# Kernel tuning notes

Measured on AMD Instinct MI355X. Metric: run time of the kernel, lower is better.

## Reference

```python
import jax, jax.numpy as jnp
import numpy as np

NUM_CLASSES = 10
EPS = 1e-6


def setup_inputs() -> dict:
    key = jax.random.key(0)
    k1, k2, k3, k4 = jax.random.split(key, 4)
    M, N, D = 4096, 32768, 512
    return {
        "x": jax.random.normal(k1, (M, D), dtype=jnp.float32),
        "x_ref": jax.random.normal(k2, (N, D), dtype=jnp.float32),
        "y": jax.random.randint(k3, (M,), 0, NUM_CLASSES),
        "y_ref": jax.random.randint(k4, (N,), 0, NUM_CLASSES),
    }


def reference(x, x_ref, y, y_ref):
    x2 = jnp.sum(x * x, axis=1)            # [M]
    r2 = jnp.sum(x_ref * x_ref, axis=1)    # [N]
    dist = jnp.sqrt(x2[:, None] - 2.0 * (x @ x_ref.T) + r2[None, :])  # [M,N]
    # scores = -distance, softmax over reference set (temperature = 1)
    score = jax.nn.softmax(-dist, axis=1)  # [M,N]
    # per-class segment sum over reference columns (replaces python loop over 10 classes)
    soft_nns = jax.ops.segment_sum(score.T, y_ref, num_segments=NUM_CLASSES).T + EPS  # [M,10]
    log_soft_nns = jnp.log(soft_nns)
    # nll_loss with reduction='mean'
    loss = -jnp.mean(jnp.take_along_axis(log_soft_nns, y[:, None], axis=1)[:, 0])
    return loss
```

## Files before the change

### kernel.cpp

```cpp
#include <hip/hip_runtime.h>
#include <hip/hip_bf16.h>
#include <stdint.h>

#define M_ROWS 4096
#define N_REFS 32768
#define DIM    512
#define NSPLIT 32
#define BM     128
#define CHUNK  128
#define SLICE  (N_REFS / NSPLIT)
#define NCHUNKS (SLICE / CHUNK)
#define NKT    (DIM / 128)
#define NSTEP  (NCHUNKS * NKT)

typedef __attribute__((ext_vector_type(4))) int   i32x4;
typedef __attribute__((ext_vector_type(8))) int   i32x8;
typedef __attribute__((ext_vector_type(4))) float f32x4;

#define C_L2E2 2.0813689810056077f

__device__ __forceinline__ uint32_t f32_to_e4m3(float f) {
  uint32_t u = __float_as_uint(f);
  uint32_t s = (u >> 24) & 0x80u;
  float a = fabsf(f);
  if (a > 448.f) a = 448.f;
  uint32_t b;
  if (a >= 0.015625f) {
    uint32_t v = __float_as_uint(a);
    v += 0x7FFFFu + ((v >> 20) & 1u);
    int e = (int)(v >> 23) - 127;
    uint32_t m = (v >> 20) & 7u;
    b = (uint32_t)((e + 7) << 3) | m;
    if (b > 0x7Eu) b = 0x7Eu;
  } else {
    b = (uint32_t)(a * 512.f + 0.5f);
  }
  return s | b;
}

__global__ void prep_rows_fp8(const float* __restrict__ src, uint8_t* __restrict__ dst,
                              float* __restrict__ sq) {
  int row = blockIdx.x;
  int t = threadIdx.x;
  const float2* s = (const float2*)(src + (size_t)row * DIM);
  float2 v = s[t];
  uint32_t p = f32_to_e4m3(v.x) | (f32_to_e4m3(v.y) << 8);
  ((uint16_t*)(dst + (size_t)row * DIM))[t] = (uint16_t)p;
  float ss = v.x * v.x + v.y * v.y;
  #pragma unroll
  for (int d = 32; d >= 1; d >>= 1) ss += __shfl_down(ss, d, 64);
  __shared__ float wsum[4];
  int w = t >> 6, lane = t & 63;
  if (lane == 0) wsum[w] = ss;
  __syncthreads();
  if (t == 0) sq[row] = C_L2E2 * (wsum[0] + wsum[1] + wsum[2] + wsum[3]);
}

__global__ __launch_bounds__(256, 2) void ask_main(
    const uint8_t* __restrict__ xf8, const uint8_t* __restrict__ rf8,
    const float* __restrict__ cx2, const float* __restrict__ cr2,
    const int* __restrict__ y, const int* __restrict__ yref,
    float* __restrict__ totG, float* __restrict__ matchG)
{
  __shared__ unsigned char smem[2 * 32768];

  const int tid  = threadIdx.x;
  const int w    = tid >> 6, lane = tid & 63;
  const int wr   = w >> 1,  wc   = w & 1;
  const int l15  = lane & 15, l4 = lane >> 4;

  const int bm       = blockIdx.x * BM;
  const int colstart = blockIdx.y * SLICE;

  const int srow = w * 8 + (lane >> 3);
  const int qsl  = lane & 7;
  const int esl  = qsl ^ (srow & 7);
  const int gsl  = (esl < 4) ? (2 * esl) : (2 * (esl & 3) + 1);
  const int scol = gsl * 16;
  const uint8_t* gA0 = xf8 + (size_t)(bm + srow) * DIM + scol;
  const uint8_t* gBb = rf8 + (size_t)(colstart + srow) * DIM + scol;

#define GLL(srcp, dstoff)                                                        \
  __builtin_amdgcn_global_load_lds(                                              \
      (const __attribute__((address_space(1))) void*)(srcp),                     \
      (__attribute__((address_space(3))) void*)(smem + (dstoff)), 16, 0, 0)

#define STAGE(gidx)                                                              \
  { const int ch_ = (gidx) >> 2, dk_ = ((gidx) & 3) * 128, b_ = ((gidx) & 1) * 32768; \
    const uint8_t* gA_ = gA0 + dk_;                                              \
    const uint8_t* gB_ = gBb + (size_t)ch_ * CHUNK * DIM + dk_;                  \
    _Pragma("unroll")                                                            \
    for (int cc = 0; cc < 4; ++cc) {                                             \
      GLL(gA_ + (size_t)cc * 32 * DIM, b_ + cc * 4096 + w * 1024);               \
      GLL(gB_ + (size_t)cc * 32 * DIM, b_ + 16384 + cc * 4096 + w * 1024);       \
    } }

  const int h   = l15 & 7;
  const int sl0 = (l4 ^ h) * 16;
  const int sl1 = sl0 ^ 64;
  int aoff[4], boff[4];
  #pragma unroll
  for (int i = 0; i < 4; ++i) {
    aoff[i] = (wr * 64 + i * 16 + l15) * 128;
    boff[i] = (wc * 64 + i * 16 + l15) * 128 + 16384;
  }

  float x2v[16]; int yv[16];
  #pragma unroll
  for (int i = 0; i < 16; ++i) {
    int row = bm + wr * 64 + (i >> 2) * 16 + l4 * 4 + (i & 3);
    x2v[i] = cx2[row];
    yv[i]  = y[row];
  }

  float tot[16], mat[16];
  #pragma unroll
  for (int i = 0; i < 16; ++i) { tot[i] = 0.f; mat[i] = 0.f; }

  f32x4 acc[4][4];
  const f32x4 fz = {0.f, 0.f, 0.f, 0.f};

  STAGE(0);
  asm volatile("s_waitcnt vmcnt(0)" ::: "memory");
  __builtin_amdgcn_s_barrier();

  #pragma unroll
  for (int g = 0; g < NSTEP; ++g) {
    const int kt = g & 3, ch = g >> 2;
    const int bofs = (g & 1) * 32768;

    if (g + 1 < NSTEP) { STAGE(g + 1); }

    if (kt == 0) {
      #pragma unroll
      for (int mi = 0; mi < 4; ++mi)
        #pragma unroll
        for (int ni = 0; ni < 4; ++ni) acc[mi][ni] = fz;
    }

    const unsigned char* pS = smem + bofs;
    i32x8 bfr[4];
    #pragma unroll
    for (int ni = 0; ni < 4; ++ni) {
      i32x4 lo = *(const i32x4*)(pS + boff[ni] + sl0);
      i32x4 hi = *(const i32x4*)(pS + boff[ni] + sl1);
      bfr[ni] = __builtin_shufflevector(lo, hi, 0, 1, 2, 3, 4, 5, 6, 7);
    }
    #pragma unroll
    for (int mi = 0; mi < 4; ++mi) {
      i32x4 lo = *(const i32x4*)(pS + aoff[mi] + sl0);
      i32x4 hi = *(const i32x4*)(pS + aoff[mi] + sl1);
      i32x8 afr = __builtin_shufflevector(lo, hi, 0, 1, 2, 3, 4, 5, 6, 7);
      #pragma unroll
      for (int ni = 0; ni < 4; ++ni)
        acc[mi][ni] = __builtin_amdgcn_mfma_scale_f32_16x16x128_f8f6f4(
            afr, bfr[ni], acc[mi][ni],
            0, 0,
            0, 0x7F7F7F7F,
            0, 0x7F7F7F7F);
    }

    if (kt == 3) {
      const int colb = colstart + ch * CHUNK;
      float r2c[4]; int cls[4];
      #pragma unroll
      for (int ni = 0; ni < 4; ++ni) {
        int cg = colb + wc * 64 + ni * 16 + l15;
        r2c[ni] = cr2[cg];
        cls[ni] = yref[cg];
      }
      #pragma unroll
      for (int mi = 0; mi < 4; ++mi) {
        #pragma unroll
        for (int r = 0; r < 4; ++r) {
          const int gi = mi * 4 + r;
          float xr = x2v[gi];
          int   yy = yv[gi];
          float tsum = 0.f, msum = 0.f;
          #pragma unroll
          for (int ni = 0; ni < 4; ++ni) {
            float t = fmaf(-2.0f * C_L2E2, acc[mi][ni][r], xr + r2c[ni]);
            t = fmaxf(t, 0.0f);
            float d = __builtin_amdgcn_sqrtf(t);
            float e = __builtin_amdgcn_exp2f(-d);
            tsum += e;
            msum = fmaf(e, (cls[ni] == yy) ? 1.0f : 0.0f, msum);
          }
          tot[gi] += tsum;
          mat[gi] += msum;
        }
      }
    }

    asm volatile("s_waitcnt vmcnt(0)" ::: "memory");
    __builtin_amdgcn_s_barrier();
  }

  #pragma unroll
  for (int i = 0; i < 16; ++i) {
    float t = tot[i], m = mat[i];
    #pragma unroll
    for (int d = 1; d <= 8; d <<= 1) {
      t += __shfl_xor(t, d, 64);
      m += __shfl_xor(m, d, 64);
    }
    if (l15 == 0) {
      int row = bm + wr * 64 + (i >> 2) * 16 + l4 * 4 + (i & 3);
      atomicAdd(&totG[row], t);
      atomicAdd(&matchG[row], m);
    }
  }
#undef GLL
#undef STAGE
}

__global__ void finalize_loss(const float* __restrict__ totG, const float* __restrict__ matchG,
                              float* __restrict__ out) {
  __shared__ float red[256];
  int t = threadIdx.x;
  float s = 0.f;
  for (int r = t; r < M_ROWS; r += 256)
    s += logf(matchG[r] / totG[r] + 1e-6f);
  red[t] = s;
  __syncthreads();
  for (int off = 128; off >= 1; off >>= 1) {
    if (t < off) red[t] += red[t + off];
    __syncthreads();
  }
  if (t == 0) out[0] = -red[0] / (float)M_ROWS;
}

extern "C" void kernel_launch(void* const* d_in, const int* in_sizes, int n_in,
                              void* d_out, int out_size, void* d_ws, size_t ws_size,
                              hipStream_t stream) {
  const float* x    = (const float*)d_in[0];
  const float* xref = (const float*)d_in[1];
  const int*   y    = (const int*)d_in[2];
  const int*   yref = (const int*)d_in[3];
  float* out = (float*)d_out;

  uint8_t* ws = (uint8_t*)d_ws;
  uint8_t* xf8    = ws;
  uint8_t* rf8    = ws + 2097152;
  float*   cx2    = (float*)(ws + 18874368);
  float*   cr2    = (float*)(ws + 18890752);
  float*   totG   = (float*)(ws + 19021824);
  float*   matchG = (float*)(ws + 19038208);

  hipMemsetAsync(totG, 0, 2 * M_ROWS * sizeof(float), stream);

  prep_rows_fp8<<<M_ROWS, 256, 0, stream>>>(x, xf8, cx2);
  prep_rows_fp8<<<N_REFS, 256, 0, stream>>>(xref, rf8, cr2);
  ask_main<<<dim3(M_ROWS / BM, NSPLIT), 256, 0, stream>>>(xf8, rf8, cx2, cr2, y, yref, totG, matchG);
  finalize_loss<<<1, 256, 0, stream>>>(totG, matchG, out);
}
```

Baseline: 139.7 us.

## Load B fragments directly from global, remap grid, fuse prep kernels

```diff
diff --git a/kernel.cpp b/kernel.cpp
--- a/kernel.cpp
+++ b/kernel.cpp
@@ -12,6 +12,7 @@
 #define NCHUNKS (SLICE / CHUNK)
 #define NKT    (DIM / 128)
 #define NSTEP  (NCHUNKS * NKT)
+#define ABUF   16384
 
 typedef __attribute__((ext_vector_type(4))) int   i32x4;
 typedef __attribute__((ext_vector_type(8))) int   i32x8;
@@ -38,9 +39,13 @@
   return s | b;
 }
 
-__global__ void prep_rows_fp8(const float* __restrict__ src, uint8_t* __restrict__ dst,
-                              float* __restrict__ sq) {
-  int row = blockIdx.x;
+__global__ void prep_all_fp8(const float* __restrict__ x, const float* __restrict__ xref,
+                             uint8_t* __restrict__ xf8, uint8_t* __restrict__ rf8,
+                             float* __restrict__ cx2, float* __restrict__ cr2) {
+  const int b = blockIdx.x;
+  const float* src; uint8_t* dst; float* sq; int row;
+  if (b < M_ROWS) { src = x;    dst = xf8; sq = cx2; row = b; }
+  else            { src = xref; dst = rf8; sq = cr2; row = b - M_ROWS; }
   int t = threadIdx.x;
   const float2* s = (const float2*)(src + (size_t)row * DIM);
   float2 v = s[t];
@@ -62,23 +67,24 @@
     const int* __restrict__ y, const int* __restrict__ yref,
     float* __restrict__ totG, float* __restrict__ matchG)
 {
-  __shared__ unsigned char smem[2 * 32768];
+  __shared__ unsigned char smem[2 * ABUF];
 
   const int tid  = threadIdx.x;
   const int w    = tid >> 6, lane = tid & 63;
   const int wr   = w >> 1,  wc   = w & 1;
   const int l15  = lane & 15, l4 = lane >> 4;
 
-  const int bm       = blockIdx.x * BM;
-  const int colstart = blockIdx.y * SLICE;
+  const int wg    = blockIdx.x;
+  const int mtile = (wg >> 3) & 31;
+  const int nsl   = (wg & 7) * 4 + (wg >> 8);
+  const int bm       = mtile * BM;
+  const int colstart = nsl * SLICE;
 
   const int srow = w * 8 + (lane >> 3);
   const int qsl  = lane & 7;
   const int esl  = qsl ^ (srow & 7);
   const int gsl  = (esl < 4) ? (2 * esl) : (2 * (esl & 3) + 1);
-  const int scol = gsl * 16;
-  const uint8_t* gA0 = xf8 + (size_t)(bm + srow) * DIM + scol;
-  const uint8_t* gBb = rf8 + (size_t)(colstart + srow) * DIM + scol;
+  const uint8_t* gA0 = xf8 + (size_t)(bm + srow) * DIM + gsl * 16;
 
 #define GLL(srcp, dstoff)                                                        \
   __builtin_amdgcn_global_load_lds(                                              \
@@ -86,24 +92,23 @@
       (__attribute__((address_space(3))) void*)(smem + (dstoff)), 16, 0, 0)
 
 #define STAGE(gidx)                                                              \
-  { const int ch_ = (gidx) >> 2, dk_ = ((gidx) & 3) * 128, b_ = ((gidx) & 1) * 32768; \
-    const uint8_t* gA_ = gA0 + dk_;                                              \
-    const uint8_t* gB_ = gBb + (size_t)ch_ * CHUNK * DIM + dk_;                  \
+  { const int dk_ = ((gidx) & 3) * 128, b_ = ((gidx) & 1) * ABUF;                \
     _Pragma("unroll")                                                            \
-    for (int cc = 0; cc < 4; ++cc) {                                             \
-      GLL(gA_ + (size_t)cc * 32 * DIM, b_ + cc * 4096 + w * 1024);               \
-      GLL(gB_ + (size_t)cc * 32 * DIM, b_ + 16384 + cc * 4096 + w * 1024);       \
-    } }
+    for (int cc = 0; cc < 4; ++cc)                                               \
+      GLL(gA0 + (size_t)cc * 32 * DIM + dk_, b_ + cc * 4096 + w * 1024); }
 
   const int h   = l15 & 7;
   const int sl0 = (l4 ^ h) * 16;
   const int sl1 = sl0 ^ 64;
-  int aoff[4], boff[4];
-  #pragma unroll
-  for (int i = 0; i < 4; ++i) {
+  int aoff[4];
+  #pragma unroll
+  for (int i = 0; i < 4; ++i)
     aoff[i] = (wr * 64 + i * 16 + l15) * 128;
-    boff[i] = (wc * 64 + i * 16 + l15) * 128 + 16384;
-  }
+
+  const uint8_t* pB0 = rf8 + (size_t)(colstart + wc * 64 + 0 * 16 + l15) * DIM + l4 * 32;
+  const uint8_t* pB1 = rf8 + (size_t)(colstart + wc * 64 + 1 * 16 + l15) * DIM + l4 * 32;
+  const uint8_t* pB2 = rf8 + (size_t)(colstart + wc * 64 + 2 * 16 + l15) * DIM + l4 * 32;
+  const uint8_t* pB3 = rf8 + (size_t)(colstart + wc * 64 + 3 * 16 + l15) * DIM + l4 * 32;
 
   float x2v[16]; int yv[16];
   #pragma unroll
@@ -119,6 +124,7 @@
 
   f32x4 acc[4][4];
   const f32x4 fz = {0.f, 0.f, 0.f, 0.f};
+  float r2cP[4]; int clsP[4];
 
   STAGE(0);
   asm volatile("s_waitcnt vmcnt(0)" ::: "memory");
@@ -127,7 +133,8 @@
   #pragma unroll
   for (int g = 0; g < NSTEP; ++g) {
     const int kt = g & 3, ch = g >> 2;
-    const int bofs = (g & 1) * 32768;
+    const int dkb = kt * 128;
+    const int bofs = (g & 1) * ABUF;
 
     if (g + 1 < NSTEP) { STAGE(g + 1); }
 
@@ -137,15 +144,30 @@
         #pragma unroll
         for (int ni = 0; ni < 4; ++ni) acc[mi][ni] = fz;
     }
+    if (kt == 2) {
+      const int colb = colstart + ch * CHUNK;
+      #pragma unroll
+      for (int ni = 0; ni < 4; ++ni) {
+        int cg = colb + wc * 64 + ni * 16 + l15;
+        r2cP[ni] = cr2[cg];
+        clsP[ni] = yref[cg];
+      }
+    }
+
+    i32x8 bfr[4];
+    {
+      i32x4 lo, hi;
+      lo = *(const i32x4*)(pB0 + dkb); hi = *(const i32x4*)(pB0 + dkb + 16);
+      bfr[0] = __builtin_shufflevector(lo, hi, 0, 1, 2, 3, 4, 5, 6, 7);
+      lo = *(const i32x4*)(pB1 + dkb); hi = *(const i32x4*)(pB1 + dkb + 16);
+      bfr[1] = __builtin_shufflevector(lo, hi, 0, 1, 2, 3, 4, 5, 6, 7);
+      lo = *(const i32x4*)(pB2 + dkb); hi = *(const i32x4*)(pB2 + dkb + 16);
+      bfr[2] = __builtin_shufflevector(lo, hi, 0, 1, 2, 3, 4, 5, 6, 7);
+      lo = *(const i32x4*)(pB3 + dkb); hi = *(const i32x4*)(pB3 + dkb + 16);
+      bfr[3] = __builtin_shufflevector(lo, hi, 0, 1, 2, 3, 4, 5, 6, 7);
+    }
 
     const unsigned char* pS = smem + bofs;
-    i32x8 bfr[4];
-    #pragma unroll
-    for (int ni = 0; ni < 4; ++ni) {
-      i32x4 lo = *(const i32x4*)(pS + boff[ni] + sl0);
-      i32x4 hi = *(const i32x4*)(pS + boff[ni] + sl1);
-      bfr[ni] = __builtin_shufflevector(lo, hi, 0, 1, 2, 3, 4, 5, 6, 7);
-    }
     #pragma unroll
     for (int mi = 0; mi < 4; ++mi) {
       i32x4 lo = *(const i32x4*)(pS + aoff[mi] + sl0);
@@ -161,14 +183,6 @@
     }
 
     if (kt == 3) {
-      const int colb = colstart + ch * CHUNK;
-      float r2c[4]; int cls[4];
-      #pragma unroll
-      for (int ni = 0; ni < 4; ++ni) {
-        int cg = colb + wc * 64 + ni * 16 + l15;
-        r2c[ni] = cr2[cg];
-        cls[ni] = yref[cg];
-      }
       #pragma unroll
       for (int mi = 0; mi < 4; ++mi) {
         #pragma unroll
@@ -179,17 +193,18 @@
           float tsum = 0.f, msum = 0.f;
           #pragma unroll
           for (int ni = 0; ni < 4; ++ni) {
-            float t = fmaf(-2.0f * C_L2E2, acc[mi][ni][r], xr + r2c[ni]);
+            float t = fmaf(-2.0f * C_L2E2, acc[mi][ni][r], xr + r2cP[ni]);
             t = fmaxf(t, 0.0f);
             float d = __builtin_amdgcn_sqrtf(t);
             float e = __builtin_amdgcn_exp2f(-d);
             tsum += e;
-            msum = fmaf(e, (cls[ni] == yy) ? 1.0f : 0.0f, msum);
+            msum = fmaf(e, (clsP[ni] == yy) ? 1.0f : 0.0f, msum);
           }
           tot[gi] += tsum;
           mat[gi] += msum;
         }
       }
+      pB0 += CHUNK * DIM; pB1 += CHUNK * DIM; pB2 += CHUNK * DIM; pB3 += CHUNK * DIM;
     }
 
     asm volatile("s_waitcnt vmcnt(0)" ::: "memory");
@@ -249,8 +264,7 @@
 
   hipMemsetAsync(totG, 0, 2 * M_ROWS * sizeof(float), stream);
 
-  prep_rows_fp8<<<M_ROWS, 256, 0, stream>>>(x, xf8, cx2);
-  prep_rows_fp8<<<N_REFS, 256, 0, stream>>>(xref, rf8, cr2);
-  ask_main<<<dim3(M_ROWS / BM, NSPLIT), 256, 0, stream>>>(xf8, rf8, cx2, cr2, y, yref, totG, matchG);
+  prep_all_fp8<<<M_ROWS + N_REFS, 256, 0, stream>>>(x, xref, xf8, rf8, cx2, cr2);
+  ask_main<<<(M_ROWS / BM) * NSPLIT, 256, 0, stream>>>(xf8, rf8, cx2, cr2, y, yref, totG, matchG);
   finalize_loss<<<1, 256, 0, stream>>>(totG, matchG, out);
 }
```

Measured after the change: 203.1 us. 1.45x slower.
